# Performance work log

Measured on AMD Instinct MI355X. Metric: run time of the kernel, lower is better.

## Reference

```python
import jax, jax.numpy as jnp
import numpy as np

# column-index constants for the node feature matrix and edge attributes
VM, VA, PG, QG, PD, QD = 0, 1, 2, 3, 4, 5
G_COL, B_COL = 0, 1

N_NODES = 100000
N_EDGES = 3200000
N_FEAT = 6


def setup_inputs() -> dict:
    key = jax.random.key(0)
    k1, k2, k3, k4, k5, k6 = jax.random.split(key, 6)
    pred = jax.random.normal(k1, (N_NODES, N_FEAT), dtype=jnp.float32)
    target = jax.random.normal(k2, (N_NODES, N_FEAT), dtype=jnp.float32)
    src = jax.random.randint(k3, (N_EDGES,), 0, N_NODES, dtype=jnp.int32)
    dst = jax.random.randint(k4, (N_EDGES,), 0, N_NODES, dtype=jnp.int32)
    edge_index = jnp.stack([src, dst], axis=0)
    edge_attr = jax.random.normal(k5, (N_EDGES, 2), dtype=jnp.float32)
    mask = jax.random.bernoulli(k6, 0.5, (N_NODES, N_FEAT))
    return {"pred": pred, "target": target, "edge_index": edge_index,
            "edge_attr": edge_attr, "mask": mask}


def reference(pred, target, edge_index, edge_attr, mask):
    # temp_pred[~mask] = target[~mask]
    tp = jnp.where(mask, pred, target)

    V_m = tp[:, VM]
    V_a = tp[:, VA]
    V = V_m * jnp.exp(1j * V_a)           # complex64 [N]
    V_conj = jnp.conj(V)

    # conj(Y_bus) entries on edges: G - jB
    Y_conj = edge_attr[:, G_COL] - 1j * edge_attr[:, B_COL]  # complex64 [E]

    row, col = edge_index[0], edge_index[1]
    # (Y_bus_conj @ V_conj)[i] = sum over edges (i,j) of conj(Y_ij) * conj(V_j)
    msg = Y_conj * V_conj[col]                               # gather-multiply [E]
    matvec = jax.ops.segment_sum(msg, row, num_segments=tp.shape[0])  # scatter-add [N]

    S_injection = V * matvec                                  # diag(V) @ (...)

    net_P = tp[:, PG] - tp[:, PD]
    net_Q = tp[:, QG] - tp[:, QD]
    diff = (net_P + 1j * net_Q) - S_injection

    loss = jnp.mean(jnp.abs(diff))
    real_loss = jnp.mean(jnp.abs(jnp.real(diff)))
    imag_loss = jnp.mean(jnp.abs(jnp.imag(diff)))
    return (loss, real_loss, imag_loss)
```

## Files before the change

kernel.cpp:

```cpp
#include <hip/hip_runtime.h>
#include <hip/hip_fp16.h>
#include <math.h>

constexpr int N_NODES = 100000;
constexpr int N_EDGES = 3200000;
constexpr int NF      = 6;

constexpr int NB      = 256;
constexpr int NMAXB   = 392;
constexpr int CAP     = 13312;
constexpr int KREC    = CAP / 1024;
constexpr int TILE    = 2048;
constexpr int EPT     = TILE / 256;
constexpr int NBLK_PART = (N_EDGES + TILE - 1) / TILE;
constexpr int VPREP_BLOCKS = (N_NODES + 255) / 256;

__device__ __forceinline__ unsigned bucket_of(int r) {
    return (unsigned)(((unsigned long long)((unsigned)r << 8) * 351843721ull) >> 45);
}
__device__ __forceinline__ int base_of(unsigned b) {
    return (int)((b * 100000u + 255u) >> 8);
}

constexpr size_t OFF_V    = 0;
constexpr size_t OFF_REC  = OFF_V + (size_t)N_NODES * 8;
constexpr size_t OFF_CNT  = OFF_REC + (size_t)NB * CAP * 8;
constexpr size_t WS_NEED  = OFF_CNT + 2048;

__device__ __forceinline__ float2 half2u_to_f2(unsigned u) {
    __half2 h;
    *reinterpret_cast<unsigned*>(&h) = u;
    return __half22float2(h);
}

__global__ __launch_bounds__(256) void partition_edges(
        const int* __restrict__ row, const int* __restrict__ col,
        const float2* __restrict__ attr,
        const float* __restrict__ pred, const float* __restrict__ target,
        const unsigned char* __restrict__ mask,
        float2* __restrict__ v_out,
        unsigned int* __restrict__ gcur,
        uint2* __restrict__ rec_g) {
    __shared__ unsigned int h[4][NB];
    __shared__ unsigned int cur[4][NB];
    __shared__ int wb[4][NB];
    __shared__ int dbase[NB];
    __shared__ unsigned int wsum_s[4];
    __shared__ uint2 rec_s[TILE];
    __shared__ unsigned char bkt_s[TILE];
    __shared__ int total_s;

    const int tid = threadIdx.x;
    const int w = tid >> 6;
    const int e0 = blockIdx.x * TILE;
    const int e_base = e0 + tid * EPT;
    const bool ok = e_base < N_EDGES;

    if (blockIdx.x < VPREP_BLOCKS) {
        int i = blockIdx.x * 256 + tid;
        if (i < N_NODES) {
            const int bb = i * NF;
            float vm = mask[bb + 0] ? pred[bb + 0] : target[bb + 0];
            float va = mask[bb + 1] ? pred[bb + 1] : target[bb + 1];
            float sn, cs;
            sincosf(va, &sn, &cs);
            v_out[i] = make_float2(vm * cs, vm * sn);
        }
    }

    for (int i = tid; i < 4 * NB; i += 256) {
        (&h[0][0])[i] = 0u;
        (&cur[0][0])[i] = 0u;
    }
    __syncthreads();

    int r[EPT];
    unsigned bk[EPT];
    if (ok) {
        int4 ra = *(const int4*)(row + e_base);
        int4 rb = *(const int4*)(row + e_base + 4);
        r[0]=ra.x; r[1]=ra.y; r[2]=ra.z; r[3]=ra.w;
        r[4]=rb.x; r[5]=rb.y; r[6]=rb.z; r[7]=rb.w;
        #pragma unroll
        for (int k = 0; k < EPT; ++k) {
            bk[k] = bucket_of(r[k]);
            atomicAdd(&h[w][bk[k]], 1u);
        }
    }
    __syncthreads();

    {
        unsigned tot = h[0][tid] + h[1][tid] + h[2][tid] + h[3][tid];
        unsigned incl = tot;
        #pragma unroll
        for (int off = 1; off < 64; off <<= 1) {
            unsigned n = __shfl_up(incl, off, 64);
            if ((tid & 63) >= off) incl += n;
        }
        if ((tid & 63) == 63) wsum_s[w] = incl;
        __syncthreads();
        unsigned woff = 0;
        if (w > 0) woff += wsum_s[0];
        if (w > 1) woff += wsum_s[1];
        if (w > 2) woff += wsum_s[2];
        incl += woff;
        int lbase = (int)(incl - tot);
        unsigned t0 = h[0][tid], t1 = h[1][tid], t2 = h[2][tid];
        unsigned g = tot ? atomicAdd(&gcur[tid], tot) : 0u;
        dbase[tid] = (int)g - lbase;
        wb[0][tid] = lbase;
        wb[1][tid] = lbase + (int)t0;
        wb[2][tid] = lbase + (int)(t0 + t1);
        wb[3][tid] = lbase + (int)(t0 + t1 + t2);
        if (tid == NB - 1) total_s = (int)incl;
    }
    __syncthreads();

    if (ok) {
        int4 ca = *(const int4*)(col + e_base);
        int4 cb = *(const int4*)(col + e_base + 4);
        int c[EPT] = {ca.x, ca.y, ca.z, ca.w, cb.x, cb.y, cb.z, cb.w};
        float4 a0 = *(const float4*)(attr + e_base);
        float4 a1 = *(const float4*)(attr + e_base + 2);
        float4 a2 = *(const float4*)(attr + e_base + 4);
        float4 a3 = *(const float4*)(attr + e_base + 6);
        float gx[EPT] = {a0.x, a0.z, a1.x, a1.z, a2.x, a2.z, a3.x, a3.z};
        float gy[EPT] = {a0.y, a0.w, a1.y, a1.w, a2.y, a2.w, a3.y, a3.w};
        #pragma unroll
        for (int k = 0; k < EPT; ++k) {
            unsigned b = bk[k];
            unsigned li = (unsigned)(r[k] - base_of(b));
            int slot = wb[w][b] + (int)atomicAdd(&cur[w][b], 1u);
            __half2 hh = __floats2half2_rn(gx[k], gy[k]);
            rec_s[slot] = make_uint2((unsigned)c[k] | (li << 17),
                                     *reinterpret_cast<unsigned int*>(&hh));
            bkt_s[slot] = (unsigned char)b;
        }
    }
    __syncthreads();

    const int total = total_s;
    for (int j = tid; j < total; j += 256) {
        int b = (int)bkt_s[j];
        int g = dbase[b] + j;
        if (g < CAP)
            rec_g[(size_t)b * CAP + g] = rec_s[j];
    }
}

__global__ __launch_bounds__(1024) void accum_bucket(
        const unsigned int* __restrict__ gcur,
        const uint2* __restrict__ rec,
        const float2* __restrict__ v,
        const float* __restrict__ pred,
        const float* __restrict__ target,
        const unsigned char* __restrict__ mask,
        float* __restrict__ sums,
        unsigned int* __restrict__ done_all,
        float* __restrict__ out) {
    __shared__ float acc_re[NMAXB];
    __shared__ float acc_im[NMAXB];
    const int tid = threadIdx.x;
    const int b = blockIdx.x;
    const int cnt = (int)min(gcur[b], (unsigned)CAP);
    if (tid < NMAXB) { acc_re[tid] = 0.f; acc_im[tid] = 0.f; }
    __syncthreads();
    const uint2* rp = rec + (size_t)b * CAP;

    uint2 q[KREC];
    #pragma unroll
    for (int k = 0; k < KREC; ++k)
        q[k] = rp[tid + (k << 10)];

    float2 vv[KREC];
    #pragma unroll
    for (int k = 0; k < KREC; ++k) {
        int idx = tid + (k << 10);
        unsigned c = (idx < cnt) ? (q[k].x & 0x1FFFFu) : 0u;
        vv[k] = v[c];
    }

    #pragma unroll
    for (int k = 0; k < KREC; ++k) {
        int idx = tid + (k << 10);
        if (idx < cnt) {
            int li = (int)(q[k].x >> 17);
            float2 gb = half2u_to_f2(q[k].y);
            float2 vk = vv[k];
            atomicAdd(&acc_re[li], fmaf(gb.x, vk.x, -gb.y * vk.y));
            atomicAdd(&acc_im[li], -fmaf(gb.x, vk.y, gb.y * vk.x));
        }
    }
    __syncthreads();

    const int base = base_of((unsigned)b);
    const int nb_nodes = base_of((unsigned)b + 1) - base;
    float a = 0.f, ar = 0.f, ai = 0.f;
    if (tid < nb_nodes) {
        int i = base + tid;
        float mr = acc_re[tid];
        float mi = acc_im[tid];
        const int bb = i * NF;
        uchar2 m23 = *(const uchar2*)(mask + bb + 2);
        uchar2 m45 = *(const uchar2*)(mask + bb + 4);
        float2 p23 = *(const float2*)(pred + bb + 2);
        float2 p45 = *(const float2*)(pred + bb + 4);
        float2 t23 = *(const float2*)(target + bb + 2);
        float2 t45 = *(const float2*)(target + bb + 4);
        float pg = m23.x ? p23.x : t23.x;
        float qg = m23.y ? p23.y : t23.y;
        float pd = m45.x ? p45.x : t45.x;
        float qd = m45.y ? p45.y : t45.y;
        float2 vv2 = v[i];
        float s_re = vv2.x * mr - vv2.y * mi;
        float s_im = vv2.x * mi + vv2.y * mr;
        float dre = (pg - pd) - s_re;
        float dim = (qg - qd) - s_im;
        ar = fabsf(dre);
        ai = fabsf(dim);
        a  = sqrtf(dre * dre + dim * dim);
    }
    #pragma unroll
    for (int off = 32; off > 0; off >>= 1) {
        a  += __shfl_down(a,  off, 64);
        ar += __shfl_down(ar, off, 64);
        ai += __shfl_down(ai, off, 64);
    }
    __shared__ float red[3][16];
    int wave = tid >> 6;
    int lane = tid & 63;
    if (lane == 0) { red[0][wave] = a; red[1][wave] = ar; red[2][wave] = ai; }
    __syncthreads();
    if (tid == 0) {
        float s0 = 0.f, s1 = 0.f, s2 = 0.f;
        #pragma unroll
        for (int k = 0; k < 16; ++k) { s0 += red[0][k]; s1 += red[1][k]; s2 += red[2][k]; }
        float r0 = atomicAdd(&sums[0], s0);
        float r1 = atomicAdd(&sums[1], s1);
        float r2 = atomicAdd(&sums[2], s2);
        float chk = r0 + r1 + r2;
        if (chk == chk) {
            unsigned fin = atomicAdd(done_all, 1u);
            if (fin == (unsigned)(NB - 1)) {
                const float inv = 1.0f / (float)N_NODES;
                float t0 = atomicAdd(&sums[0], 0.f);
                float t1 = atomicAdd(&sums[1], 0.f);
                float t2 = atomicAdd(&sums[2], 0.f);
                __hip_atomic_store(&out[0], t0 * inv, __ATOMIC_RELAXED, __HIP_MEMORY_SCOPE_AGENT);
                __hip_atomic_store(&out[1], t1 * inv, __ATOMIC_RELAXED, __HIP_MEMORY_SCOPE_AGENT);
                __hip_atomic_store(&out[2], t2 * inv, __ATOMIC_RELAXED, __HIP_MEMORY_SCOPE_AGENT);
            }
        }
    }
}

__global__ void node_prep_fb(const float* __restrict__ pred,
                             const float* __restrict__ target,
                             const unsigned char* __restrict__ mask,
                             float2* __restrict__ v) {
    int i = blockIdx.x * blockDim.x + threadIdx.x;
    if (i >= N_NODES) return;
    const int b = i * NF;
    float vm = mask[b + 0] ? pred[b + 0] : target[b + 0];
    float va = mask[b + 1] ? pred[b + 1] : target[b + 1];
    float s, c;
    sincosf(va, &s, &c);
    v[i] = make_float2(vm * c, vm * s);
}

__global__ void edge_scatter_fb(const int* __restrict__ row,
                                const int* __restrict__ col,
                                const float2* __restrict__ attr,
                                const float2* __restrict__ v,
                                float2* __restrict__ mv) {
    int e = blockIdx.x * blockDim.x + threadIdx.x;
    if (e >= N_EDGES) return;
    int r = row[e];
    int c = col[e];
    float2 gb = attr[e];
    float2 vv = v[c];
    float mre = fmaf(gb.x, vv.x, -gb.y * vv.y);
    float mim = -fmaf(gb.x, vv.y, gb.y * vv.x);
    atomicAdd(&mv[r].x, mre);
    atomicAdd(&mv[r].y, mim);
}

__global__ void finalize_fb(const float* __restrict__ pred,
                            const float* __restrict__ target,
                            const unsigned char* __restrict__ mask,
                            const float2* __restrict__ v,
                            const float2* __restrict__ mv,
                            float* __restrict__ sums) {
    int i = blockIdx.x * blockDim.x + threadIdx.x;
    float a = 0.f, ar = 0.f, ai = 0.f;
    if (i < N_NODES) {
        const int b = i * NF;
        float pg = mask[b + 2] ? pred[b + 2] : target[b + 2];
        float qg = mask[b + 3] ? pred[b + 3] : target[b + 3];
        float pd = mask[b + 4] ? pred[b + 4] : target[b + 4];
        float qd = mask[b + 5] ? pred[b + 5] : target[b + 5];
        float netP = pg - pd;
        float netQ = qg - qd;
        float2 vv = v[i];
        float2 m = mv[i];
        float s_re = vv.x * m.x - vv.y * m.y;
        float s_im = vv.x * m.y + vv.y * m.x;
        float dre = netP - s_re;
        float dim = netQ - s_im;
        ar = fabsf(dre);
        ai = fabsf(dim);
        a  = sqrtf(dre * dre + dim * dim);
    }
    #pragma unroll
    for (int off = 32; off > 0; off >>= 1) {
        a  += __shfl_down(a,  off, 64);
        ar += __shfl_down(ar, off, 64);
        ai += __shfl_down(ai, off, 64);
    }
    __shared__ float red[3][4];
    int wave = threadIdx.x >> 6;
    int lane = threadIdx.x & 63;
    if (lane == 0) { red[0][wave] = a; red[1][wave] = ar; red[2][wave] = ai; }
    __syncthreads();
    if (threadIdx.x == 0) {
        atomicAdd(&sums[0], red[0][0] + red[0][1] + red[0][2] + red[0][3]);
        atomicAdd(&sums[1], red[1][0] + red[1][1] + red[1][2] + red[1][3]);
        atomicAdd(&sums[2], red[2][0] + red[2][1] + red[2][2] + red[2][3]);
    }
}

__global__ void write_out_fb(const float* __restrict__ sums, float* __restrict__ out) {
    if (threadIdx.x == 0 && blockIdx.x == 0) {
        const float inv = 1.0f / (float)N_NODES;
        out[0] = sums[0] * inv;
        out[1] = sums[1] * inv;
        out[2] = sums[2] * inv;
    }
}

extern "C" void kernel_launch(void* const* d_in, const int* in_sizes, int n_in,
                              void* d_out, int out_size, void* d_ws, size_t ws_size,
                              hipStream_t stream) {
    const float*         pred   = (const float*)d_in[0];
    const float*         target = (const float*)d_in[1];
    const int*           eidx   = (const int*)d_in[2];
    const float2*        attr   = (const float2*)d_in[3];
    const unsigned char* mask   = (const unsigned char*)d_in[4];
    float* out = (float*)d_out;

    const int* row = eidx;
    const int* col = eidx + N_EDGES;

    char* ws = (char*)d_ws;
    const int B = 256;

    if (ws_size >= WS_NEED) {
        float2*       v        = (float2*)(ws + OFF_V);
        uint2*        rec_g    = (uint2*)(ws + OFF_REC);
        unsigned int* gcur     = (unsigned int*)(ws + OFF_CNT);
        float*        sums     = (float*)(ws + OFF_CNT + 1536);
        unsigned int* done_all = (unsigned int*)(ws + OFF_CNT + 1552);

        hipMemsetAsync(ws + OFF_CNT, 0, 2048, stream);
        partition_edges<<<NBLK_PART, B, 0, stream>>>(row, col, attr,
                                                     pred, target, mask, v,
                                                     gcur, rec_g);
        accum_bucket<<<NB, 1024, 0, stream>>>(gcur, rec_g, v,
                                              pred, target, mask,
                                              sums, done_all, out);
    } else {
        float2* v    = (float2*)ws;
        float2* mv   = (float2*)(ws + (size_t)N_NODES * 8);
        float*  sums = (float*)(ws + 2ull * N_NODES * 8);
        hipMemsetAsync(mv, 0, (size_t)N_NODES * 8 + 16, stream);
        node_prep_fb<<<(N_NODES + B - 1) / B, B, 0, stream>>>(pred, target, mask, v);
        edge_scatter_fb<<<(N_EDGES + B - 1) / B, B, 0, stream>>>(row, col, attr, v, mv);
        finalize_fb<<<(N_NODES + B - 1) / B, B, 0, stream>>>(pred, target, mask, v, mv, sums);
        write_out_fb<<<1, 64, 0, stream>>>(sums, out);
    }
}
```

Baseline: 187.5 us.

## Double bucket count to 512 and use single shared histogram per block

Splits the node range into 512 buckets instead of 256, halving per-bucket capacity and node count so accum_bucket launches twice as many smaller blocks with fewer records per thread. The partition kernel drops per-wave histograms in favour of one shared histogram, with each thread scanning two buckets. This aims to raise occupancy and parallelism in the accumulation phase, in exchange for more shared-atomic contention and more global scatter destinations during partitioning.

```diff
diff --git a/kernel.cpp b/kernel.cpp
--- a/kernel.cpp
+++ b/kernel.cpp
@@ -6,9 +6,9 @@
 constexpr int N_EDGES = 3200000;
 constexpr int NF      = 6;
 
-constexpr int NB      = 256;
-constexpr int NMAXB   = 392;
-constexpr int CAP     = 13312;
+constexpr int NB      = 512;
+constexpr int NMAXB   = 196;
+constexpr int CAP     = 7168;
 constexpr int KREC    = CAP / 1024;
 constexpr int TILE    = 2048;
 constexpr int EPT     = TILE / 256;
@@ -16,16 +16,16 @@
 constexpr int VPREP_BLOCKS = (N_NODES + 255) / 256;
 
 __device__ __forceinline__ unsigned bucket_of(int r) {
-    return (unsigned)(((unsigned long long)((unsigned)r << 8) * 351843721ull) >> 45);
+    return (unsigned)(((unsigned long long)((unsigned)r << 9) * 351843721ull) >> 45);
 }
 __device__ __forceinline__ int base_of(unsigned b) {
-    return (int)((b * 100000u + 255u) >> 8);
+    return (int)((b * 100000u + 511u) >> 9);
 }
 
 constexpr size_t OFF_V    = 0;
 constexpr size_t OFF_REC  = OFF_V + (size_t)N_NODES * 8;
 constexpr size_t OFF_CNT  = OFF_REC + (size_t)NB * CAP * 8;
-constexpr size_t WS_NEED  = OFF_CNT + 2048;
+constexpr size_t WS_NEED  = OFF_CNT + 4096;
 
 __device__ __forceinline__ float2 half2u_to_f2(unsigned u) {
     __half2 h;
@@ -41,13 +41,13 @@
         float2* __restrict__ v_out,
         unsigned int* __restrict__ gcur,
         uint2* __restrict__ rec_g) {
-    __shared__ unsigned int h[4][NB];
-    __shared__ unsigned int cur[4][NB];
-    __shared__ int wb[4][NB];
+    __shared__ unsigned int h[NB];
+    __shared__ unsigned int cur[NB];
+    __shared__ int sbase[NB];
     __shared__ int dbase[NB];
     __shared__ unsigned int wsum_s[4];
     __shared__ uint2 rec_s[TILE];
-    __shared__ unsigned char bkt_s[TILE];
+    __shared__ unsigned short bkt_s[TILE];
     __shared__ int total_s;
 
     const int tid = threadIdx.x;
@@ -68,10 +68,8 @@
         }
     }
 
-    for (int i = tid; i < 4 * NB; i += 256) {
-        (&h[0][0])[i] = 0u;
-        (&cur[0][0])[i] = 0u;
-    }
+    h[tid] = 0u;  h[tid + 256] = 0u;
+    cur[tid] = 0u; cur[tid + 256] = 0u;
     __syncthreads();
 
     int r[EPT];
@@ -84,14 +82,16 @@
         #pragma unroll
         for (int k = 0; k < EPT; ++k) {
             bk[k] = bucket_of(r[k]);
-            atomicAdd(&h[w][bk[k]], 1u);
+            atomicAdd(&h[bk[k]], 1u);
         }
     }
     __syncthreads();
 
     {
-        unsigned tot = h[0][tid] + h[1][tid] + h[2][tid] + h[3][tid];
-        unsigned incl = tot;
+        int b0 = 2 * tid, b1 = 2 * tid + 1;
+        unsigned c0 = h[b0], c1 = h[b1];
+        unsigned pair = c0 + c1;
+        unsigned incl = pair;
         #pragma unroll
         for (int off = 1; off < 64; off <<= 1) {
             unsigned n = __shfl_up(incl, off, 64);
@@ -103,16 +103,14 @@
         if (w > 0) woff += wsum_s[0];
         if (w > 1) woff += wsum_s[1];
         if (w > 2) woff += wsum_s[2];
-        incl += woff;
-        int lbase = (int)(incl - tot);
-        unsigned t0 = h[0][tid], t1 = h[1][tid], t2 = h[2][tid];
-        unsigned g = tot ? atomicAdd(&gcur[tid], tot) : 0u;
-        dbase[tid] = (int)g - lbase;
-        wb[0][tid] = lbase;
-        wb[1][tid] = lbase + (int)t0;
-        wb[2][tid] = lbase + (int)(t0 + t1);
-        wb[3][tid] = lbase + (int)(t0 + t1 + t2);
-        if (tid == NB - 1) total_s = (int)incl;
+        unsigned excl = woff + incl - pair;
+        sbase[b0] = (int)excl;
+        sbase[b1] = (int)(excl + c0);
+        unsigned g0 = c0 ? atomicAdd(&gcur[b0], c0) : 0u;
+        unsigned g1 = c1 ? atomicAdd(&gcur[b1], c1) : 0u;
+        dbase[b0] = (int)g0 - (int)excl;
+        dbase[b1] = (int)g1 - (int)(excl + c0);
+        if (tid == 255) total_s = (int)(woff + incl);
     }
     __syncthreads();
 
@@ -130,11 +128,11 @@
         for (int k = 0; k < EPT; ++k) {
             unsigned b = bk[k];
             unsigned li = (unsigned)(r[k] - base_of(b));
-            int slot = wb[w][b] + (int)atomicAdd(&cur[w][b], 1u);
+            int slot = sbase[b] + (int)atomicAdd(&cur[b], 1u);
             __half2 hh = __floats2half2_rn(gx[k], gy[k]);
             rec_s[slot] = make_uint2((unsigned)c[k] | (li << 17),
                                      *reinterpret_cast<unsigned int*>(&hh));
-            bkt_s[slot] = (unsigned char)b;
+            bkt_s[slot] = (unsigned short)b;
         }
     }
     __syncthreads();
@@ -171,7 +169,6 @@
     #pragma unroll
     for (int k = 0; k < KREC; ++k)
         q[k] = rp[tid + (k << 10)];
-
     float2 vv[KREC];
     #pragma unroll
     for (int k = 0; k < KREC; ++k) {
@@ -179,7 +176,6 @@
         unsigned c = (idx < cnt) ? (q[k].x & 0x1FFFFu) : 0u;
         vv[k] = v[c];
     }
-
     #pragma unroll
     for (int k = 0; k < KREC; ++k) {
         int idx = tid + (k << 10);
@@ -358,10 +354,10 @@
         float2*       v        = (float2*)(ws + OFF_V);
         uint2*        rec_g    = (uint2*)(ws + OFF_REC);
         unsigned int* gcur     = (unsigned int*)(ws + OFF_CNT);
-        float*        sums     = (float*)(ws + OFF_CNT + 1536);
-        unsigned int* done_all = (unsigned int*)(ws + OFF_CNT + 1552);
-
-        hipMemsetAsync(ws + OFF_CNT, 0, 2048, stream);
+        float*        sums     = (float*)(ws + OFF_CNT + 2048);
+        unsigned int* done_all = (unsigned int*)(ws + OFF_CNT + 2064);
+
+        hipMemsetAsync(ws + OFF_CNT, 0, 4096, stream);
         partition_edges<<<NBLK_PART, B, 0, stream>>>(row, col, attr,
                                                      pred, target, mask, v,
                                                      gcur, rec_g);
```

Result: slower. 214.0 us (+14.2%).

## Move V gather and complex multiply into partition pass, storing products

Applied to the files above, without the earlier changes.

Node voltage prep moves into its own kernel that runs before partitioning. The partition kernel then gathers V[col] and computes the complex product conj(Y)*conj(V) per edge, storing a half2 message plus the local row index. The accumulate kernel no longer does a random gather from V and only sums the precomputed messages. In exchange there is an extra kernel launch and the gather moves into the partition phase, and rounding the product rather than the admittance to half precision changes numerical error.

```diff
diff --git a/kernel.cpp b/kernel.cpp
--- a/kernel.cpp
+++ b/kernel.cpp
@@ -33,12 +33,28 @@
     return __half22float2(h);
 }
 
+__global__ __launch_bounds__(256) void node_prep(
+        const float* __restrict__ pred,
+        const float* __restrict__ target,
+        const unsigned char* __restrict__ mask,
+        float2* __restrict__ v) {
+    int i = blockIdx.x * 256 + threadIdx.x;
+    if (i >= N_NODES) return;
+    const int b = i * NF;
+    uchar2 m01 = *(const uchar2*)(mask + b);
+    float2 p01 = *(const float2*)(pred + b);
+    float2 t01 = *(const float2*)(target + b);
+    float vm = m01.x ? p01.x : t01.x;
+    float va = m01.y ? p01.y : t01.y;
+    float s, c;
+    sincosf(va, &s, &c);
+    v[i] = make_float2(vm * c, vm * s);
+}
+
 __global__ __launch_bounds__(256) void partition_edges(
         const int* __restrict__ row, const int* __restrict__ col,
         const float2* __restrict__ attr,
-        const float* __restrict__ pred, const float* __restrict__ target,
-        const unsigned char* __restrict__ mask,
-        float2* __restrict__ v_out,
+        const float2* __restrict__ v,
         unsigned int* __restrict__ gcur,
         uint2* __restrict__ rec_g) {
     __shared__ unsigned int h[4][NB];
@@ -55,18 +71,6 @@
     const int e0 = blockIdx.x * TILE;
     const int e_base = e0 + tid * EPT;
     const bool ok = e_base < N_EDGES;
-
-    if (blockIdx.x < VPREP_BLOCKS) {
-        int i = blockIdx.x * 256 + tid;
-        if (i < N_NODES) {
-            const int bb = i * NF;
-            float vm = mask[bb + 0] ? pred[bb + 0] : target[bb + 0];
-            float va = mask[bb + 1] ? pred[bb + 1] : target[bb + 1];
-            float sn, cs;
-            sincosf(va, &sn, &cs);
-            v_out[i] = make_float2(vm * cs, vm * sn);
-        }
-    }
 
     for (int i = tid; i < 4 * NB; i += 256) {
         (&h[0][0])[i] = 0u;
@@ -120,6 +124,9 @@
         int4 ca = *(const int4*)(col + e_base);
         int4 cb = *(const int4*)(col + e_base + 4);
         int c[EPT] = {ca.x, ca.y, ca.z, ca.w, cb.x, cb.y, cb.z, cb.w};
+        float2 vv[EPT];
+        #pragma unroll
+        for (int k = 0; k < EPT; ++k) vv[k] = v[c[k]];
         float4 a0 = *(const float4*)(attr + e_base);
         float4 a1 = *(const float4*)(attr + e_base + 2);
         float4 a2 = *(const float4*)(attr + e_base + 4);
@@ -131,9 +138,10 @@
             unsigned b = bk[k];
             unsigned li = (unsigned)(r[k] - base_of(b));
             int slot = wb[w][b] + (int)atomicAdd(&cur[w][b], 1u);
-            __half2 hh = __floats2half2_rn(gx[k], gy[k]);
-            rec_s[slot] = make_uint2((unsigned)c[k] | (li << 17),
-                                     *reinterpret_cast<unsigned int*>(&hh));
+            float mre = fmaf(gx[k], vv[k].x, -gy[k] * vv[k].y);
+            float mim = -fmaf(gx[k], vv[k].y, gy[k] * vv[k].x);
+            __half2 hh = __floats2half2_rn(mre, mim);
+            rec_s[slot] = make_uint2(*reinterpret_cast<unsigned int*>(&hh), li);
             bkt_s[slot] = (unsigned char)b;
         }
     }
@@ -167,28 +175,15 @@
     __syncthreads();
     const uint2* rp = rec + (size_t)b * CAP;
 
-    uint2 q[KREC];
-    #pragma unroll
-    for (int k = 0; k < KREC; ++k)
-        q[k] = rp[tid + (k << 10)];
-
-    float2 vv[KREC];
     #pragma unroll
     for (int k = 0; k < KREC; ++k) {
         int idx = tid + (k << 10);
-        unsigned c = (idx < cnt) ? (q[k].x & 0x1FFFFu) : 0u;
-        vv[k] = v[c];
-    }
-
-    #pragma unroll
-    for (int k = 0; k < KREC; ++k) {
-        int idx = tid + (k << 10);
+        uint2 q = rp[idx];
         if (idx < cnt) {
-            int li = (int)(q[k].x >> 17);
-            float2 gb = half2u_to_f2(q[k].y);
-            float2 vk = vv[k];
-            atomicAdd(&acc_re[li], fmaf(gb.x, vk.x, -gb.y * vk.y));
-            atomicAdd(&acc_im[li], -fmaf(gb.x, vk.y, gb.y * vk.x));
+            float2 m = half2u_to_f2(q.x);
+            int li = (int)q.y;
+            atomicAdd(&acc_re[li], m.x);
+            atomicAdd(&acc_im[li], m.y);
         }
     }
     __syncthreads();
@@ -362,8 +357,8 @@
         unsigned int* done_all = (unsigned int*)(ws + OFF_CNT + 1552);
 
         hipMemsetAsync(ws + OFF_CNT, 0, 2048, stream);
-        partition_edges<<<NBLK_PART, B, 0, stream>>>(row, col, attr,
-                                                     pred, target, mask, v,
+        node_prep<<<VPREP_BLOCKS, B, 0, stream>>>(pred, target, mask, v);
+        partition_edges<<<NBLK_PART, B, 0, stream>>>(row, col, attr, v,
                                                      gcur, rec_g);
         accum_bucket<<<NB, 1024, 0, stream>>>(gcur, rec_g, v,
                                               pred, target, mask,
```

New measurement: 192.7 us. 1.03x slower.
